# Kernel tuning notes

Hardware: AMD Instinct MI355X
Metric: run time of the kernel (lower is better)

The kernel has to match this reference:

```python
import jax, jax.numpy as jnp
import numpy as np

SEQ_LEN = 15
BATCH = 32
N_NODES = 5000
N_EDGES = 80000
IN_FEAT = 16
NHID = 2
G_FEAT = 1
HIDDEN = 512
N_LAYERS = 2


def setup_inputs() -> dict:
    key = jax.random.key(0)
    ks = jax.random.split(key, 16)
    x = jax.random.normal(ks[0], (SEQ_LEN, BATCH, N_NODES, IN_FEAT), dtype=jnp.float32)
    edge_index = jax.random.randint(ks[1], (2, N_EDGES), 0, N_NODES, dtype=jnp.int64)
    # per-timestep GCN weights (one GCN per timestep in the torch module)
    W1 = jax.random.normal(ks[2], (SEQ_LEN, IN_FEAT, NHID), dtype=jnp.float32) / np.sqrt(IN_FEAT)
    b1 = jnp.zeros((SEQ_LEN, NHID), dtype=jnp.float32)
    W2 = jax.random.normal(ks[3], (SEQ_LEN, NHID, G_FEAT), dtype=jnp.float32) / np.sqrt(NHID)
    b2 = jnp.zeros((SEQ_LEN, G_FEAT), dtype=jnp.float32)
    rnn_in = G_FEAT * N_NODES
    s_in = 1.0 / np.sqrt(HIDDEN)
    w_ih0 = jax.random.uniform(ks[4], (3 * HIDDEN, rnn_in), jnp.float32, -s_in, s_in)
    w_hh0 = jax.random.uniform(ks[5], (3 * HIDDEN, HIDDEN), jnp.float32, -s_in, s_in)
    b_ih0 = jax.random.uniform(ks[6], (3 * HIDDEN,), jnp.float32, -s_in, s_in)
    b_hh0 = jax.random.uniform(ks[7], (3 * HIDDEN,), jnp.float32, -s_in, s_in)
    w_ih1 = jax.random.uniform(ks[8], (3 * HIDDEN, HIDDEN), jnp.float32, -s_in, s_in)
    w_hh1 = jax.random.uniform(ks[9], (3 * HIDDEN, HIDDEN), jnp.float32, -s_in, s_in)
    b_ih1 = jax.random.uniform(ks[10], (3 * HIDDEN,), jnp.float32, -s_in, s_in)
    b_hh1 = jax.random.uniform(ks[11], (3 * HIDDEN,), jnp.float32, -s_in, s_in)
    return {"x": x, "edge_index": edge_index, "W1": W1, "b1": b1, "W2": W2, "b2": b2,
            "w_ih0": w_ih0, "w_hh0": w_hh0, "b_ih0": b_ih0, "b_hh0": b_hh0,
            "w_ih1": w_ih1, "w_hh1": w_hh1, "b_ih1": b_ih1, "b_hh1": b_hh1}


def _gcn_norm(edge_index, n_nodes):
    # PyG GCNConv: add self-loops, symmetric normalization
    loop = jnp.arange(n_nodes, dtype=edge_index.dtype)
    row = jnp.concatenate([edge_index[0], loop])  # source
    col = jnp.concatenate([edge_index[1], loop])  # target
    deg = jnp.zeros((n_nodes,), jnp.float32).at[col].add(1.0)
    dinv = deg ** -0.5  # deg >= 1 thanks to self-loops
    norm = dinv[row] * dinv[col]  # [E+N]
    return row, col, norm


def _propagate(h, row, col, norm, n_nodes):
    # h: [S,B,N,C] -> gather sources, scale, scatter-add to targets
    m = norm[:, None] * jnp.take(h, row, axis=2)  # [S,B,E,C]
    return jnp.zeros(h.shape[:2] + (n_nodes, h.shape[-1]), h.dtype).at[:, :, col, :].add(m)


def _gru_layer(inp, w_ih, w_hh, b_ih, b_hh):
    # inp: [S,B,I]; torch GRU cell math
    H = w_hh.shape[1]
    gi = jnp.einsum('sbi,gi->sbg', inp, w_ih) + b_ih  # [S,B,3H], precomputed input gates
    h0 = jnp.zeros((inp.shape[1], H), inp.dtype)

    def step(h, gi_t):
        gh = h @ w_hh.T + b_hh
        ir, iz, inn = jnp.split(gi_t, 3, axis=-1)
        hr, hz, hn = jnp.split(gh, 3, axis=-1)
        r = jax.nn.sigmoid(ir + hr)
        z = jax.nn.sigmoid(iz + hz)
        n = jnp.tanh(inn + r * hn)
        h_new = (1.0 - z) * n + z * h
        return h_new, h_new

    h_last, out = jax.lax.scan(step, h0, gi)
    return out, h_last


def reference(x, edge_index, W1, b1, W2, b2,
              w_ih0, w_hh0, b_ih0, b_hh0, w_ih1, w_hh1, b_ih1, b_hh1):
    S, B, N, F = x.shape
    row, col, norm = _gcn_norm(edge_index, N)
    # conv1: linear (per-timestep weights) -> propagate -> bias -> relu (dropout inactive in eval)
    h = jnp.einsum('sbnf,sfh->sbnh', x, W1)
    h = _propagate(h, row, col, norm, N) + b1[:, None, None, :]
    h = jax.nn.relu(h)
    # conv2
    h = jnp.einsum('sbnh,sho->sbno', h, W2)
    h = _propagate(h, row, col, norm, N) + b2[:, None, None, :]
    g = jnp.tanh(h).reshape(S, B, N * h.shape[-1])  # [S,B,rnn_in]
    out1, h1 = _gru_layer(g, w_ih0, w_hh0, b_ih0, b_hh0)
    out2, h2 = _gru_layer(out1, w_ih1, w_hh1, b_ih1, b_hh1)
    hn = jnp.stack([h1, h2])  # [n_layers,B,H]
    return out2, hn
```

## Files before the change

### kernel.cpp

```cpp
#include <hip/hip_runtime.h>

typedef unsigned int uint_t;

#define SEQ 15
#define BATCH 32
#define NNODES 5000
#define NEDGES 80000
#define INFEAT 16
#define HID 512
#define G3 1536
#define GRU_BLOCKS 256
#define BAR_INTS (32 * (2 * GRU_BLOCKS))

#define KSPLIT 9
#define KCHUNK 576
#define MROWS 480
#define LDSP 68

#define NSLC 16
#define PPAD 36

#define NT64 ((NNODES + 63) / 64)

__device__ __forceinline__ float sigmoidf(float x){ return 1.0f / (1.0f + __expf(-x)); }

__global__ void k_init(int* counts, int* fill, int* bar,
                       float* h0a, float* h0b, float* h1a, float* h1b){
    int t = blockIdx.x * 256 + threadIdx.x;
    if (t < NNODES){ counts[t] = 0; fill[t] = 0; }
    if (t < BAR_INTS) bar[t] = 0;
    h0a[t] = 0.f; h0b[t] = 0.f; h1a[t] = 0.f; h1b[t] = 0.f;
}

__global__ void k_count(const int* ei, int* counts){
    int e = blockIdx.x * 256 + threadIdx.x;
    if (e < NEDGES) atomicAdd(&counts[ei[NEDGES + e]], 1);
}

__global__ void k_dinv(const int* counts, float* dinv){
    int n = blockIdx.x * 256 + threadIdx.x;
    if (n < NNODES) dinv[n] = rsqrtf(1.0f + (float)counts[n]);
}

__global__ void k_scan(const int* counts, int* offs){
    __shared__ int sdata[1024];
    int tid = threadIdx.x;
    int base = tid * 5;
    int loc[5]; int tot = 0;
    #pragma unroll
    for (int q = 0; q < 5; q++){
        int idx = base + q;
        int v = (idx < NNODES) ? counts[idx] : 0;
        loc[q] = tot; tot += v;
    }
    sdata[tid] = tot; __syncthreads();
    for (int off = 1; off < 1024; off <<= 1){
        int t = (tid >= off) ? sdata[tid - off] : 0;
        __syncthreads();
        sdata[tid] += t;
        __syncthreads();
    }
    int excl = sdata[tid] - tot;
    #pragma unroll
    for (int q = 0; q < 5; q++){
        int idx = base + q;
        if (idx < NNODES) offs[idx] = excl + loc[q];
    }
    if (tid == 1023) offs[NNODES] = sdata[1023];
}

__global__ void k_fill(const int* ei, const int* offs, int* fill, int* csr){
    int e = blockIdx.x * 256 + threadIdx.x;
    if (e < NEDGES){
        int c = ei[NEDGES + e];
        int p = offs[c] + atomicAdd(&fill[c], 1);
        csr[p] = ei[e];
    }
}

__global__ __launch_bounds__(256) void k_conv1(const float* __restrict__ x,
        const float* __restrict__ W1, const float* __restrict__ dinv,
        float* __restrict__ h1t){
    int s = blockIdx.y;
    int nn = threadIdx.x & 63;
    int n  = blockIdx.x * 64 + nn;
    int bq = threadIdx.x >> 6;
    if (n >= NNODES) return;
    float w[32];
    #pragma unroll
    for (int q = 0; q < 32; q++) w[q] = W1[s * 32 + q];
    float d = dinv[n];
    size_t sbase = (size_t)s * NNODES;
    for (int j = 0; j < 8; j++){
        int b = bq * 8 + j;
        const float4* xp = (const float4*)(x + ((size_t)(s * BATCH + b) * NNODES + n) * INFEAT);
        float4 u0 = xp[0], u1 = xp[1], u2 = xp[2], u3 = xp[3];
        float xs[16] = { u0.x,u0.y,u0.z,u0.w, u1.x,u1.y,u1.z,u1.w,
                         u2.x,u2.y,u2.z,u2.w, u3.x,u3.y,u3.z,u3.w };
        float a0 = 0.f, a1 = 0.f;
        #pragma unroll
        for (int f = 0; f < 16; f++){ a0 += xs[f] * w[2 * f]; a1 += xs[f] * w[2 * f + 1]; }
        ((float2*)h1t)[(sbase + n) * 32 + b] = make_float2(d * a0, d * a1);
    }
}

__global__ __launch_bounds__(256) void k_agg1(const float* __restrict__ h1t,
        const int* __restrict__ offs, const int* __restrict__ csr,
        const float* __restrict__ dinv, const float* __restrict__ b1,
        const float* __restrict__ W2, float* __restrict__ h2t){
    int s = blockIdx.y;
    int n0 = blockIdx.x * 64;
    int wv = threadIdx.x >> 6, l = threadIdx.x & 63;
    float w20 = W2[s * 2 + 0], w21 = W2[s * 2 + 1];
    float bb1 = b1[s * 2 + (l & 1)];
    size_t sbase = (size_t)s * NNODES;
    for (int r = 0; r < 16; r++){
        int n = n0 + wv + 4 * r;
        if (n >= NNODES) continue;
        const float* hp = h1t + (sbase + n) * 64;
        float acc = hp[l];
        int e0 = offs[n], e1 = offs[n + 1];
        for (int p = e0; p < e1; p++){
            int src = csr[p];
            acc += h1t[(sbase + src) * 64 + l];
        }
        float d = dinv[n];
        float val = fmaxf(d * acc + bb1, 0.f);
        float oth = __shfl_xor(val, 1);
        if ((l & 1) == 0)
            h2t[(sbase + n) * 32 + (l >> 1)] = d * (val * w20 + oth * w21);
    }
}

__global__ __launch_bounds__(256) void k_agg2(const float* __restrict__ h2t,
        const int* __restrict__ offs, const int* __restrict__ csr,
        const float* __restrict__ dinv, const float* __restrict__ b2,
        float* __restrict__ g){
    __shared__ float gst[64 * 33];
    int s = blockIdx.y;
    int n0 = blockIdx.x * 64;
    int wv = threadIdx.x >> 6, l = threadIdx.x & 63;
    int half = l >> 5, bl = l & 31;
    float bs = b2[s];
    size_t sbase = (size_t)s * NNODES;
    for (int r = 0; r < 16; r++){
        int n = n0 + wv + 4 * r;
        if (n < NNODES){
            float acc = half ? 0.f : h2t[(sbase + n) * 32 + bl];
            int e0 = offs[n], e1 = offs[n + 1];
            for (int p = e0 + half; p < e1; p += 2){
                int src = csr[p];
                acc += h2t[(sbase + src) * 32 + bl];
            }
            acc += __shfl_xor(acc, 32);
            if (half == 0)
                gst[(wv + 4 * r) * 33 + bl] = tanhf(dinv[n] * acc + bs);
        }
    }
    __syncthreads();
    #pragma unroll
    for (int q = 0; q < 8; q++){
        int flat = q * 256 + threadIdx.x;
        int b = flat >> 6, nn = flat & 63;
        int n = n0 + nn;
        if (n < NNODES)
            g[((size_t)s * BATCH + b) * NNODES + n] = gst[nn * 33 + b];
    }
}

__global__ __launch_bounds__(256) void k_gemm(const float* A, const float* W,
                                              float* part){
    __shared__ float As[16 * LDSP];
    __shared__ float Bs[16 * LDSP];
    int tid = threadIdx.x;
    int j0 = blockIdx.x * 64;
    int m0 = blockIdx.y * 64;
    int kz = blockIdx.z;
    int kbeg = kz * KCHUNK;
    int kend = kbeg + KCHUNK; if (kend > 5000) kend = 5000;
    int tm = tid >> 4, tn = tid & 15;
    int lr = tid >> 2;
    int lk = (tid & 3) * 4;
    float acc[4][4];
    #pragma unroll
    for (int i = 0; i < 4; i++)
        #pragma unroll
        for (int j = 0; j < 4; j++) acc[i][j] = 0.f;

    for (int k0 = kbeg; k0 < kend; k0 += 16){
        int m = m0 + lr;
        float4 av = make_float4(0.f, 0.f, 0.f, 0.f);
        if (m < MROWS && (k0 + lk) < 5000)
            av = *(const float4*)&A[(size_t)m * 5000 + k0 + lk];
        As[(lk + 0) * LDSP + lr] = av.x; As[(lk + 1) * LDSP + lr] = av.y;
        As[(lk + 2) * LDSP + lr] = av.z; As[(lk + 3) * LDSP + lr] = av.w;
        int j = j0 + lr;
        float4 bv = make_float4(0.f, 0.f, 0.f, 0.f);
        if ((k0 + lk) < 5000)
            bv = *(const float4*)&W[(size_t)j * 5000 + k0 + lk];
        Bs[(lk + 0) * LDSP + lr] = bv.x; Bs[(lk + 1) * LDSP + lr] = bv.y;
        Bs[(lk + 2) * LDSP + lr] = bv.z; Bs[(lk + 3) * LDSP + lr] = bv.w;
        __syncthreads();
        #pragma unroll
        for (int k = 0; k < 16; k++){
            float4 a = *(float4*)&As[k * LDSP + tm * 4];
            float4 bb = *(float4*)&Bs[k * LDSP + tn * 4];
            acc[0][0] += a.x * bb.x; acc[0][1] += a.x * bb.y; acc[0][2] += a.x * bb.z; acc[0][3] += a.x * bb.w;
            acc[1][0] += a.y * bb.x; acc[1][1] += a.y * bb.y; acc[1][2] += a.y * bb.z; acc[1][3] += a.y * bb.w;
            acc[2][0] += a.z * bb.x; acc[2][1] += a.z * bb.y; acc[2][2] += a.z * bb.z; acc[2][3] += a.z * bb.w;
            acc[3][0] += a.w * bb.x; acc[3][1] += a.w * bb.y; acc[3][2] += a.w * bb.z; acc[3][3] += a.w * bb.w;
        }
        __syncthreads();
    }
    size_t zbase = (size_t)kz * MROWS * G3;
    #pragma unroll
    for (int i = 0; i < 4; i++){
        int m = m0 + tm * 4 + i;
        if (m < MROWS){
            #pragma unroll
            for (int j = 0; j < 4; j++){
                int col = j0 + tn * 4 + j;
                part[zbase + (size_t)m * G3 + col] = acc[i][j];
            }
        }
    }
}

__global__ __launch_bounds__(256) void k_gred(const float* part, const float* bias, float* C){
    int idx = blockIdx.x * 256 + threadIdx.x;
    float s = bias[idx % G3];
    float sum = 0.f;
    #pragma unroll
    for (int z = 0; z < KSPLIT; z++)
        sum += part[(size_t)z * MROWS * G3 + idx];
    C[idx] = sum + s;
}

__device__ __forceinline__ void grid_barrier(int* bar, int phase){
    __syncthreads();
    if (threadIdx.x == 0){
        __threadfence();
        __hip_atomic_store(&bar[32 * blockIdx.x], phase,
                           __ATOMIC_RELAXED, __HIP_MEMORY_SCOPE_AGENT);
    }
    if (blockIdx.x == 0 && threadIdx.x < 64){
        int lane = threadIdx.x;
        for (;;){
            int mn = 0x7fffffff;
            #pragma unroll
            for (int q = 0; q < 4; q++){
                int v = __hip_atomic_load(&bar[32 * (lane + 64 * q)],
                                          __ATOMIC_RELAXED, __HIP_MEMORY_SCOPE_AGENT);
                mn = min(mn, v);
            }
            if (__all(mn >= phase)) break;
            __builtin_amdgcn_s_sleep(4);
        }
        __threadfence();
        #pragma unroll
        for (int q = 0; q < 4; q++)
            __hip_atomic_store(&bar[32 * (GRU_BLOCKS + lane + 64 * q)], phase,
                               __ATOMIC_RELAXED, __HIP_MEMORY_SCOPE_AGENT);
    }
    if (threadIdx.x == 0){
        while (__hip_atomic_load(&bar[32 * (GRU_BLOCKS + blockIdx.x)],
                                 __ATOMIC_RELAXED, __HIP_MEMORY_SCOPE_AGENT) < phase)
            __builtin_amdgcn_s_sleep(4);
        __threadfence();
    }
    __syncthreads();
}

template<int NR>
__device__ __forceinline__ void gemv_part(const float* __restrict__ h,
                                          const float* __restrict__ wsm0,
                                          float* __restrict__ part0, int bq, int ks){
    float acc[NR][4];
    #pragma unroll
    for (int r = 0; r < NR; r++){ acc[r][0] = acc[r][1] = acc[r][2] = acc[r][3] = 0.f; }
    #pragma unroll 2
    for (int j = 0; j < 8; j++){
        int k = ks * 4 + j * 64;
        float4 hv0 = *(const float4*)&h[(k + 0) * 32 + 4 * bq];
        float4 hv1 = *(const float4*)&h[(k + 1) * 32 + 4 * bq];
        float4 hv2 = *(const float4*)&h[(k + 2) * 32 + 4 * bq];
        float4 hv3 = *(const float4*)&h[(k + 3) * 32 + 4 * bq];
        #pragma unroll
        for (int r = 0; r < NR; r++){
            float4 w = *(const float4*)&wsm0[r * HID + k];
            acc[r][0] += w.x * hv0.x + w.y * hv1.x + w.z * hv2.x + w.w * hv3.x;
            acc[r][1] += w.x * hv0.y + w.y * hv1.y + w.z * hv2.y + w.w * hv3.y;
            acc[r][2] += w.x * hv0.z + w.y * hv1.z + w.z * hv2.z + w.w * hv3.z;
            acc[r][3] += w.x * hv0.w + w.y * hv1.w + w.z * hv2.w + w.w * hv3.w;
        }
    }
    #pragma unroll
    for (int r = 0; r < NR; r++)
        *(float4*)&part0[(r * NSLC + ks) * PPAD + 4 * bq] =
            make_float4(acc[r][0], acc[r][1], acc[r][2], acc[r][3]);
}

__global__ __launch_bounds__(512, 2) void k_gru(
        const float* __restrict__ gi0,
        const float* __restrict__ wih1, const float* __restrict__ whh0,
        const float* __restrict__ whh1,
        const float* __restrict__ bih1, const float* __restrict__ bhh0,
        const float* __restrict__ bhh1,
        float* __restrict__ h0a, float* __restrict__ h0b,
        float* __restrict__ h1a, float* __restrict__ h1b,
        float* __restrict__ out, int* bar){
    __shared__ float wsm[18 * HID];
    __shared__ float part[18 * NSLC * PPAD];
    __shared__ float ghl[18 * 32];
    __shared__ float outst[SEQ * 64];

    int tid = threadIdx.x;
    int i0 = blockIdx.x * 2;

    #pragma unroll
    for (int r = 0; r < 6; r++){
        int j = (r >> 1) * HID + i0 + (r & 1);
        for (int k = tid; k < HID; k += 512){
            wsm[r * HID + k]        = whh0[(size_t)j * HID + k];
            wsm[(6 + r) * HID + k]  = wih1[(size_t)j * HID + k];
            wsm[(12 + r) * HID + k] = whh1[(size_t)j * HID + k];
        }
    }
    __syncthreads();

    int t8  = tid & 255;
    int bq  = t8 & 7;
    int ks  = (t8 >> 3) & (NSLC - 1);
    int rh  = t8 >> 7;
    int l   = (tid >> 5) & 1, bb = tid & 31;
    int i   = i0 + l;
    float hs0 = 0.f, hs1 = 0.f;

    for (int p = 0; p <= SEQ; p++){
        const float* h0r = (p & 1) ? h0a : h0b;
        float*       h0w = (p & 1) ? h0b : h0a;
        const float* h1r = (p & 1) ? h1b : h1a;
        float*       h1w = (p & 1) ? h1a : h1b;

        float giR = 0.f, giZ = 0.f, giN = 0.f;
        if (tid < 64 && p < SEQ){
            const float* gi = gi0 + (size_t)(p * BATCH + bb) * G3;
            giR = gi[i]; giZ = gi[HID + i]; giN = gi[2 * HID + i];
        }

        if (tid < 256) gemv_part<6>(h0r, wsm + (rh * 6) * HID,
                                    part + (rh * 6) * NSLC * PPAD, bq, ks);
        else           gemv_part<3>(h1r, wsm + (12 + rh * 3) * HID,
                                    part + (12 + rh * 3) * NSLC * PPAD, bq, ks);
        __syncthreads();

        for (int o = tid; o < 18 * 32; o += 512){
            int row = o >> 5, b2 = o & 31;
            float sum = 0.f;
            #pragma unroll
            for (int q = 0; q < NSLC; q++) sum += part[(row * NSLC + q) * PPAD + b2];
            ghl[row * 32 + b2] = sum;
        }
        __syncthreads();

        if (tid < 64){
            if (p < SEQ){
                float ghr = ghl[(0 + l) * 32 + bb] + bhh0[i];
                float ghz = ghl[(2 + l) * 32 + bb] + bhh0[HID + i];
                float ghn = ghl[(4 + l) * 32 + bb] + bhh0[2 * HID + i];
                float rr = sigmoidf(giR + ghr);
                float zz = sigmoidf(giZ + ghz);
                float nn = tanhf(giN + rr * ghn);
                hs0 = (1.f - zz) * nn + zz * hs0;
                h0w[i * 32 + bb] = hs0;
            }
            if (p >= 1){
                float gir = ghl[(6 + l) * 32 + bb]  + bih1[i];
                float giz = ghl[(8 + l) * 32 + bb]  + bih1[HID + i];
                float gin = ghl[(10 + l) * 32 + bb] + bih1[2 * HID + i];
                float ghr = ghl[(12 + l) * 32 + bb] + bhh1[i];
                float ghz = ghl[(14 + l) * 32 + bb] + bhh1[HID + i];
                float ghn = ghl[(16 + l) * 32 + bb] + bhh1[2 * HID + i];
                float rr = sigmoidf(gir + ghr);
                float zz = sigmoidf(giz + ghz);
                float nn = tanhf(gin + rr * ghn);
                hs1 = (1.f - zz) * nn + zz * hs1;
                h1w[i * 32 + bb] = hs1;
                outst[(p - 1) * 64 + bb * 2 + l] = hs1;
            }
        }
        if (p < SEQ) grid_barrier(bar, p + 1);
    }

    __syncthreads();
    for (int o = tid; o < SEQ * 32; o += 512){
        int q = o >> 5, b2 = o & 31;
        float2 v = *(float2*)&outst[q * 64 + b2 * 2];
        *(float2*)&out[(size_t)(q * BATCH + b2) * HID + i0] = v;
    }
    if (tid < 64){
        out[SEQ * BATCH * HID + (size_t)bb * HID + i] = hs0;
        out[SEQ * BATCH * HID + BATCH * HID + (size_t)bb * HID + i] = hs1;
    }
}

extern "C" void kernel_launch(void* const* d_in, const int* in_sizes, int n_in,
                              void* d_out, int out_size, void* d_ws, size_t ws_size,
                              hipStream_t stream){
    (void)in_sizes; (void)n_in; (void)out_size; (void)ws_size;
    const float* x    = (const float*)d_in[0];
    const int*   ei   = (const int*)d_in[1];
    const float* W1   = (const float*)d_in[2];
    const float* b1   = (const float*)d_in[3];
    const float* W2   = (const float*)d_in[4];
    const float* b2   = (const float*)d_in[5];
    const float* wih0 = (const float*)d_in[6];
    const float* whh0 = (const float*)d_in[7];
    const float* bih0 = (const float*)d_in[8];
    const float* bhh0 = (const float*)d_in[9];
    const float* wih1 = (const float*)d_in[10];
    const float* whh1 = (const float*)d_in[11];
    const float* bih1 = (const float*)d_in[12];
    const float* bhh1 = (const float*)d_in[13];
    float* out = (float*)d_out;

    char* w = (char*)d_ws;
    auto alloc = [&](size_t bytes) -> char* {
        char* p = w; w += (bytes + 255) & ~(size_t)255; return p;
    };
    float* dinv   = (float*)alloc(NNODES * 4);
    int*   counts = (int*)  alloc(NNODES * 4);
    int*   offs   = (int*)  alloc((NNODES + 8) * 4);
    int*   fill   = (int*)  alloc(NNODES * 4);
    int*   csr    = (int*)  alloc(NEDGES * 4);
    int*   bar    = (int*)  alloc(BAR_INTS * 4);
    float* h0a    = (float*)alloc(HID * BATCH * 4);
    float* h0b    = (float*)alloc(HID * BATCH * 4);
    float* h1a    = (float*)alloc(HID * BATCH * 4);
    float* h1b    = (float*)alloc(HID * BATCH * 4);
    float* h1t    = (float*)alloc((size_t)SEQ * NNODES * BATCH * 2 * 4);
    float* h2t    = (float*)alloc((size_t)SEQ * NNODES * BATCH * 4);
    float* gbuf   = (float*)alloc((size_t)SEQ * BATCH * NNODES * 4);
    float* gi0    = (float*)alloc((size_t)SEQ * BATCH * G3 * 4);
    float* part   = h1t;

    k_init <<<64, 256, 0, stream>>>(counts, fill, bar, h0a, h0b, h1a, h1b);
    k_count<<<(NEDGES + 255) / 256, 256, 0, stream>>>(ei, counts);
    k_dinv <<<(NNODES + 255) / 256, 256, 0, stream>>>(counts, dinv);
    k_scan <<<1, 1024, 0, stream>>>(counts, offs);
    k_fill <<<(NEDGES + 255) / 256, 256, 0, stream>>>(ei, offs, fill, csr);

    dim3 gtile(NT64, SEQ);
    k_conv1<<<gtile, 256, 0, stream>>>(x, W1, dinv, h1t);
    k_agg1 <<<gtile, 256, 0, stream>>>(h1t, offs, csr, dinv, b1, W2, h2t);
    k_agg2 <<<gtile, 256, 0, stream>>>(h2t, offs, csr, dinv, b2, gbuf);

    k_gemm<<<dim3(G3 / 64, 8, KSPLIT), 256, 0, stream>>>(gbuf, wih0, part);
    k_gred<<<(MROWS * G3) / 256, 256, 0, stream>>>(part, bih0, gi0);

    k_gru<<<GRU_BLOCKS, 512, 0, stream>>>(gi0, wih1, whh0, whh1, bih1, bhh0, bhh1,
                                          h0a, h0b, h1a, h1b, out, bar);
}
```

Measured before the change: 887.6 us.

## Balance GCN aggregation across edges with shared-memory atomic accumulation

The CSR now stores (source, target) pairs, and both aggregation kernels distribute all edges of a 64-node tile evenly across warps instead of assigning one node per warp. Contributions are accumulated into a shared-memory tile with LDS atomics, then bias, activation and the W2 projection or tanh are applied. This targets load imbalance from uneven node degrees and serial per-node edge loops. In exchange it adds shared-memory atomic contention, doubles the CSR size, and makes floating-point summation order nondeterministic.

```diff
diff --git a/kernel.cpp b/kernel.cpp
--- a/kernel.cpp
+++ b/kernel.cpp
@@ -69,12 +69,12 @@
     if (tid == 1023) offs[NNODES] = sdata[1023];
 }
 
-__global__ void k_fill(const int* ei, const int* offs, int* fill, int* csr){
+__global__ void k_fill(const int* ei, const int* offs, int* fill, int2* csr2){
     int e = blockIdx.x * 256 + threadIdx.x;
     if (e < NEDGES){
         int c = ei[NEDGES + e];
         int p = offs[c] + atomicAdd(&fill[c], 1);
-        csr[p] = ei[e];
+        csr2[p] = make_int2(ei[e], c);
     }
 }
 
@@ -105,62 +105,78 @@
 }
 
 __global__ __launch_bounds__(256) void k_agg1(const float* __restrict__ h1t,
-        const int* __restrict__ offs, const int* __restrict__ csr,
+        const int* __restrict__ offs, const int2* __restrict__ csr2,
         const float* __restrict__ dinv, const float* __restrict__ b1,
         const float* __restrict__ W2, float* __restrict__ h2t){
+    __shared__ float acc[64 * 64];
     int s = blockIdx.y;
     int n0 = blockIdx.x * 64;
-    int wv = threadIdx.x >> 6, l = threadIdx.x & 63;
+    int ntop = min(n0 + 64, NNODES);
+    int nloc_cnt = ntop - n0;
+    int tid = threadIdx.x;
+    int wv = tid >> 6, l = tid & 63;
+    size_t sbase = (size_t)s * NNODES;
+
+    const float* selfp = h1t + (sbase + n0) * 64;
+    for (int o = tid; o < nloc_cnt * 64; o += 256) acc[o] = selfp[o];
+    __syncthreads();
+
+    int e0 = offs[n0], e1 = offs[ntop];
+    for (int p = e0 + wv; p < e1; p += 4){
+        int2 e = csr2[p];
+        float v = h1t[(sbase + e.x) * 64 + l];
+        atomicAdd(&acc[(e.y - n0) * 64 + l], v);
+    }
+    __syncthreads();
+
     float w20 = W2[s * 2 + 0], w21 = W2[s * 2 + 1];
-    float bb1 = b1[s * 2 + (l & 1)];
-    size_t sbase = (size_t)s * NNODES;
-    for (int r = 0; r < 16; r++){
-        int n = n0 + wv + 4 * r;
-        if (n >= NNODES) continue;
-        const float* hp = h1t + (sbase + n) * 64;
-        float acc = hp[l];
-        int e0 = offs[n], e1 = offs[n + 1];
-        for (int p = e0; p < e1; p++){
-            int src = csr[p];
-            acc += h1t[(sbase + src) * 64 + l];
-        }
+    float b10 = b1[s * 2 + 0], b11 = b1[s * 2 + 1];
+    for (int o = tid; o < nloc_cnt * 32; o += 256){
+        int nloc = o >> 5, b = o & 31;
+        int n = n0 + nloc;
+        float2 a = *(float2*)&acc[nloc * 64 + 2 * b];
         float d = dinv[n];
-        float val = fmaxf(d * acc + bb1, 0.f);
-        float oth = __shfl_xor(val, 1);
-        if ((l & 1) == 0)
-            h2t[(sbase + n) * 32 + (l >> 1)] = d * (val * w20 + oth * w21);
+        float r0 = fmaxf(d * a.x + b10, 0.f);
+        float r1 = fmaxf(d * a.y + b11, 0.f);
+        h2t[(sbase + n) * 32 + b] = d * (r0 * w20 + r1 * w21);
     }
 }
 
 __global__ __launch_bounds__(256) void k_agg2(const float* __restrict__ h2t,
-        const int* __restrict__ offs, const int* __restrict__ csr,
+        const int* __restrict__ offs, const int2* __restrict__ csr2,
         const float* __restrict__ dinv, const float* __restrict__ b2,
         float* __restrict__ g){
+    __shared__ float acc2[64 * 32];
     __shared__ float gst[64 * 33];
     int s = blockIdx.y;
     int n0 = blockIdx.x * 64;
-    int wv = threadIdx.x >> 6, l = threadIdx.x & 63;
-    int half = l >> 5, bl = l & 31;
+    int ntop = min(n0 + 64, NNODES);
+    int nloc_cnt = ntop - n0;
+    int tid = threadIdx.x;
+    int hw = tid >> 5, bl = tid & 31;
+    size_t sbase = (size_t)s * NNODES;
+
+    const float* selfp = h2t + (sbase + n0) * 32;
+    for (int o = tid; o < nloc_cnt * 32; o += 256) acc2[o] = selfp[o];
+    __syncthreads();
+
+    int e0 = offs[n0], e1 = offs[ntop];
+    for (int p = e0 + hw; p < e1; p += 8){
+        int2 e = csr2[p];
+        float v = h2t[(sbase + e.x) * 32 + bl];
+        atomicAdd(&acc2[(e.y - n0) * 32 + bl], v);
+    }
+    __syncthreads();
+
     float bs = b2[s];
-    size_t sbase = (size_t)s * NNODES;
-    for (int r = 0; r < 16; r++){
-        int n = n0 + wv + 4 * r;
-        if (n < NNODES){
-            float acc = half ? 0.f : h2t[(sbase + n) * 32 + bl];
-            int e0 = offs[n], e1 = offs[n + 1];
-            for (int p = e0 + half; p < e1; p += 2){
-                int src = csr[p];
-                acc += h2t[(sbase + src) * 32 + bl];
-            }
-            acc += __shfl_xor(acc, 32);
-            if (half == 0)
-                gst[(wv + 4 * r) * 33 + bl] = tanhf(dinv[n] * acc + bs);
-        }
+    for (int o = tid; o < nloc_cnt * 32; o += 256){
+        int nloc = o >> 5, b = o & 31;
+        gst[nloc * 33 + b] = tanhf(dinv[n0 + nloc] * acc2[o] + bs);
     }
     __syncthreads();
     #pragma unroll
     for (int q = 0; q < 8; q++){
-        int flat = q * 256 + threadIdx.x;
+        int flat = q * 256 + tid;
         int b = flat >> 6, nn = flat & 63;
         int n = n0 + nn;
         if (n < NNODES)
@@ -432,7 +448,7 @@
     int*   counts = (int*)  alloc(NNODES * 4);
     int*   offs   = (int*)  alloc((NNODES + 8) * 4);
     int*   fill   = (int*)  alloc(NNODES * 4);
-    int*   csr    = (int*)  alloc(NEDGES * 4);
+    int2*  csr2   = (int2*) alloc((size_t)NEDGES * 8);
     int*   bar    = (int*)  alloc(BAR_INTS * 4);
     float* h0a    = (float*)alloc(HID * BATCH * 4);
     float* h0b    = (float*)alloc(HID * BATCH * 4);
@@ -448,12 +464,12 @@
     k_count<<<(NEDGES + 255) / 256, 256, 0, stream>>>(ei, counts);
     k_dinv <<<(NNODES + 255) / 256, 256, 0, stream>>>(counts, dinv);
     k_scan <<<1, 1024, 0, stream>>>(counts, offs);
-    k_fill <<<(NEDGES + 255) / 256, 256, 0, stream>>>(ei, offs, fill, csr);
+    k_fill <<<(NEDGES + 255) / 256, 256, 0, stream>>>(ei, offs, fill, csr2);
 
     dim3 gtile(NT64, SEQ);
     k_conv1<<<gtile, 256, 0, stream>>>(x, W1, dinv, h1t);
-    k_agg1 <<<gtile, 256, 0, stream>>>(h1t, offs, csr, dinv, b1, W2, h2t);
-    k_agg2 <<<gtile, 256, 0, stream>>>(h2t, offs, csr, dinv, b2, gbuf);
+    k_agg1 <<<gtile, 256, 0, stream>>>(h1t, offs, csr2, dinv, b1, W2, h2t);
+    k_agg2 <<<gtile, 256, 0, stream>>>(h2t, offs, csr2, dinv, b2, gbuf);
 
     k_gemm<<<dim3(G3 / 64, 8, KSPLIT), 256, 0, stream>>>(gbuf, wih0, part);
     k_gred<<<(MROWS * G3) / 256, 256, 0, stream>>>(part, bih0, gi0);
```

Measured after the change: 1.258 ms. +41.8%, slower.
